# Performance work log

Hardware: AMD Instinct MI355X
Metric: run time of the kernel (lower is better)

## Reference

```python
import jax, jax.numpy as jnp
import numpy as np

EPS = 1e-5  # BatchNorm eps
STRIDE = 10  # front_stride

def conv1d(x, w, b, stride=1, padding=0, dilation=1, groups=1):
    # x: [N,C,T], w: [O, C//groups, K] (torch OIH layout)
    y = jax.lax.conv_general_dilated(
        x, w, (stride,), [(padding, padding)], rhs_dilation=(dilation,),
        dimension_numbers=('NCH', 'OIH', 'NCH'), feature_group_count=groups)
    return y + b[None, :, None]

def bn_eval(x, g, b, m, v):
    scale = g / jnp.sqrt(v + EPS)
    return (x - m[None, :, None]) * scale[None, :, None] + b[None, :, None]

def prelu(x, a):
    return jnp.where(x > 0, x, a * x)

def setup_inputs() -> dict:
    key = jax.random.key(0)
    ks = jax.random.split(key, 12)
    B, Cin, T = 2, 1, 64000
    E, D, BL, L, K, FK = 256, 512, 2, 6, 3, 20
    s = 0.05
    x = jax.random.normal(ks[0], (B, Cin, T), dtype=jnp.float32)
    enc_w = jax.random.normal(ks[1], (E, Cin, FK), dtype=jnp.float32) * s
    enc_b = jnp.zeros((E,), jnp.float32)
    w1 = jax.random.normal(ks[2], (BL, L, D, E, 1), dtype=jnp.float32) * s
    b1 = jnp.zeros((BL, L, D), jnp.float32)
    a1 = jnp.full((BL, L), 0.25, jnp.float32)
    g1 = jnp.ones((BL, L, D), jnp.float32)
    be1 = jnp.zeros((BL, L, D), jnp.float32)
    m1 = jax.random.normal(ks[3], (BL, L, D), dtype=jnp.float32) * 0.1
    v1 = jax.random.uniform(ks[4], (BL, L, D), jnp.float32, 0.5, 1.5)
    wd = jax.random.normal(ks[5], (BL, L, D, 1, K), dtype=jnp.float32) * s
    bd = jnp.zeros((BL, L, D), jnp.float32)
    a2 = jnp.full((BL, L), 0.25, jnp.float32)
    g2 = jnp.ones((BL, L, D), jnp.float32)
    be2 = jnp.zeros((BL, L, D), jnp.float32)
    m2 = jax.random.normal(ks[6], (BL, L, D), dtype=jnp.float32) * 0.1
    v2 = jax.random.uniform(ks[7], (BL, L, D), jnp.float32, 0.5, 1.5)
    w2 = jax.random.normal(ks[8], (BL, L, E, D, 1), dtype=jnp.float32) * s
    b2 = jnp.zeros((BL, L, E), jnp.float32)
    dec_w = jax.random.normal(ks[9], (E, Cin, FK), dtype=jnp.float32) * s
    dec_b = jnp.zeros((Cin,), jnp.float32)
    return dict(x=x, enc_w=enc_w, enc_b=enc_b, w1=w1, b1=b1, a1=a1, g1=g1,
                be1=be1, m1=m1, v1=v1, wd=wd, bd=bd, a2=a2, g2=g2, be2=be2,
                m2=m2, v2=v2, w2=w2, b2=b2, dec_w=dec_w, dec_b=dec_b)

def reference(x, enc_w, enc_b, w1, b1, a1, g1, be1, m1, v1, wd, bd,
              a2, g2, be2, m2, v2, w2, b2, dec_w, dec_b):
    T = x.shape[2]
    FK = enc_w.shape[-1]
    D = wd.shape[2]
    blocks, layers = w1.shape[0], w1.shape[1]
    # encoder: Conv1d(in, E, FK, stride=10, padding=FK)
    enc = conv1d(x, enc_w, enc_b, stride=STRIDE, padding=FK)
    h = enc
    for bI in range(blocks):
        resid = h
        for i in range(layers):
            dil = 2 ** i
            h = conv1d(h, w1[bI, i], b1[bI, i])
            h = bn_eval(prelu(h, a1[bI, i]), g1[bI, i], be1[bI, i], m1[bI, i], v1[bI, i])
            h = conv1d(h, wd[bI, i], bd[bI, i], padding=dil, dilation=dil, groups=D)
            h = bn_eval(prelu(h, a2[bI, i]), g2[bI, i], be2[bI, i], m2[bI, i], v2[bI, i])
            h = conv1d(h, w2[bI, i], b2[bI, i])
        h = h + resid
    mask = jax.nn.sigmoid(h)
    masked = enc * mask
    # ConvTranspose1d(E, in, FK, stride=10, padding=0) as lhs-dilated conv
    wt = jnp.flip(dec_w, -1).transpose(1, 0, 2)  # [in, E, FK]
    dec = jax.lax.conv_general_dilated(
        masked, wt, (1,), [(FK - 1, FK - 1)], lhs_dilation=(STRIDE,),
        dimension_numbers=('NCH', 'OIH', 'NCH')) + dec_b[None, :, None]
    return dec[:, :, FK:T + FK]
```

## Files before the change

kernel.cpp:

```cpp
#include <hip/hip_runtime.h>
#include <math.h>

#define TLEN   64000
#define ECH    256
#define DCH    512
#define NBLK   2
#define NLAY   6
#define FKC    20
#define STRIDE_ 10
#define TC     6403
#define NS     12928
#define NTILE  101
#define EPSV   1e-5f

typedef __attribute__((ext_vector_type(8))) short          s8v;
typedef __attribute__((ext_vector_type(4))) float          f4v;
typedef __attribute__((ext_vector_type(4))) unsigned short u4v;
typedef __attribute__((ext_vector_type(8))) unsigned short u8v;

__device__ __forceinline__ unsigned short f2bf(float f) {
    union { float f; unsigned u; } v; v.f = f;
    unsigned r = v.u + 0x7FFFu + ((v.u >> 16) & 1u);
    return (unsigned short)(r >> 16);
}
__device__ __forceinline__ float bf2f(unsigned short h) {
    union { unsigned u; float f; } v; v.u = ((unsigned)h) << 16; return v.f;
}

#define NWQ (12*512*256/4)
__global__ __launch_bounds__(256)
void wcvt_k(const float* __restrict__ w1, const float* __restrict__ w2,
            unsigned short* __restrict__ w1b, unsigned short* __restrict__ w2b)
{
    int i = blockIdx.x * 256 + threadIdx.x;
    if (i < NWQ) {
        float4 v = ((const float4*)w1)[i];
        u4v o = { f2bf(v.x), f2bf(v.y), f2bf(v.z), f2bf(v.w) };
        ((u4v*)w1b)[i] = o;
    } else {
        int j = i - NWQ;
        float4 v = ((const float4*)w2)[j];
        u4v o = { f2bf(v.x), f2bf(v.y), f2bf(v.z), f2bf(v.w) };
        ((u4v*)w2b)[j] = o;
    }
}

__global__ __launch_bounds__(256)
void encoder_k(const float* __restrict__ x, const float* __restrict__ ew,
               const float* __restrict__ eb,
               unsigned short* __restrict__ EncB, unsigned short* __restrict__ Hb)
{
    __shared__ float xs[660];
    const int bx  = blockIdx.x;
    const int b   = blockIdx.y;
    const int tc0 = bx * 64;
    const int base_g = tc0 * STRIDE_ - FKC;
    for (int i = threadIdx.x; i < 660; i += 256) {
        int idx = base_g + i;
        xs[i] = (idx >= 0 && idx < TLEN) ? x[b * TLEN + idx] : 0.f;
    }
    __syncthreads();

    const int e = threadIdx.x;
    float w[20];
    #pragma unroll
    for (int q = 0; q < 5; ++q) {
        float4 v = *(const float4*)&ew[e * 20 + q * 4];
        w[q*4+0] = v.x; w[q*4+1] = v.y; w[q*4+2] = v.z; w[q*4+3] = v.w;
    }
    const float bz = eb[e];
    const int jmax = (TC - tc0 < 64) ? (TC - tc0) : 64;
    for (int j = 0; j < jmax; ++j) {
        const float* xp = &xs[j * 10];
        float acc = bz;
        #pragma unroll
        for (int k = 0; k < 20; ++k) acc = fmaf(xp[k], w[k], acc);
        unsigned short hv = f2bf(acc);
        size_t o = (size_t)(b * TC + tc0 + j) * 256 + e;
        EncB[o] = hv;
        Hb[o]   = hv;
    }
}

template<int KD, int MOUT, int EPI>
__global__ __launch_bounds__(256)
void gemm_bf16_k(const unsigned short* __restrict__ Wb,
                 const unsigned short* __restrict__ Act,
                 unsigned short* __restrict__ OutB,
                 const float* __restrict__ bias,
                 const float* __restrict__ alpha,
                 const float* __restrict__ gamma,
                 const float* __restrict__ beta,
                 const float* __restrict__ mean,
                 const float* __restrict__ var,
                 const unsigned short* __restrict__ Resid)
{
    __shared__ short At[2 * 128 * 32];
    __shared__ short Bt[2 * 128 * 32];

    const int t    = threadIdx.x;
    const int lane = t & 63;
    const int wid  = t >> 6;
    const int wm   = wid >> 1, wn = wid & 1;
    const int r16  = lane & 15, g = lane >> 4;
    const int mb   = blockIdx.y * 128;
    const int nb   = blockIdx.x * 128;

    f4v acc[4][4];
    #pragma unroll
    for (int a = 0; a < 4; ++a)
        #pragma unroll
        for (int c = 0; c < 4; ++c)
            acc[a][c] = (f4v){0.f, 0.f, 0.f, 0.f};

    const char* gA = (const char*)Wb;
    const char* gB = (const char*)Act;
    char* lA = (char*)At;
    char* lB = (char*)Bt;

    auto stage = [&](int buf, int k0) {
        #pragma unroll
        for (int i = 0; i < 2; ++i) {
            int ch = i * 256 + t;
            const char* srcA = gA + ((size_t)(mb + (ch >> 2)) * KD + k0) * 2 + (ch & 3) * 16;
            __builtin_amdgcn_global_load_lds(
                (const __attribute__((address_space(1))) void*)srcA,
                (__attribute__((address_space(3))) void*)(lA + buf * 8192 + i * 4096 + wid * 1024),
                16, 0, 0);
            const char* srcB = gB + ((size_t)(nb + (ch >> 2)) * KD + k0) * 2 + (ch & 3) * 16;
            __builtin_amdgcn_global_load_lds(
                (const __attribute__((address_space(1))) void*)srcB,
                (__attribute__((address_space(3))) void*)(lB + buf * 8192 + i * 4096 + wid * 1024),
                16, 0, 0);
        }
    };

    constexpr int NSTEP = KD / 32;
    stage(0, 0);
    __syncthreads();

    for (int s = 0; s < NSTEP; ++s) {
        const int cur = s & 1;
        if (s + 1 < NSTEP) stage(cur ^ 1, (s + 1) * 32);

        const short* cA = At + cur * 128 * 32;
        const short* cB = Bt + cur * 128 * 32;
        s8v av[4], bv[4];
        #pragma unroll
        for (int f = 0; f < 4; ++f) {
            av[f] = *(const s8v*)&cA[(wm * 64 + f * 16 + r16) * 32 + g * 8];
            bv[f] = *(const s8v*)&cB[(wn * 64 + f * 16 + r16) * 32 + g * 8];
        }
        #pragma unroll
        for (int fm = 0; fm < 4; ++fm)
            #pragma unroll
            for (int fn = 0; fn < 4; ++fn)
                acc[fm][fn] = __builtin_amdgcn_mfma_f32_16x16x32_bf16(
                    av[fm], bv[fn], acc[fm][fn], 0, 0, 0);

        __syncthreads();
    }

    float al = 0.f;
    if constexpr (EPI == 0) al = alpha[0];
    #pragma unroll
    for (int fm = 0; fm < 4; ++fm) {
        const int mbase = mb + wm * 64 + fm * 16 + g * 4;
        float4 b4 = *(const float4*)&bias[mbase];
        float bb[4] = { b4.x, b4.y, b4.z, b4.w };
        float sc[4], mn[4], bt[4];
        if constexpr (EPI == 0) {
            float4 g4  = *(const float4*)&gamma[mbase];
            float4 v4  = *(const float4*)&var[mbase];
            float4 m4  = *(const float4*)&mean[mbase];
            float4 be4 = *(const float4*)&beta[mbase];
            sc[0] = g4.x / sqrtf(v4.x + EPSV); sc[1] = g4.y / sqrtf(v4.y + EPSV);
            sc[2] = g4.z / sqrtf(v4.z + EPSV); sc[3] = g4.w / sqrtf(v4.w + EPSV);
            mn[0] = m4.x; mn[1] = m4.y; mn[2] = m4.z; mn[3] = m4.w;
            bt[0] = be4.x; bt[1] = be4.y; bt[2] = be4.z; bt[3] = be4.w;
        }
        #pragma unroll
        for (int fn = 0; fn < 4; ++fn) {
            const int n = nb + wn * 64 + fn * 16 + r16;
            f4v a = acc[fm][fn];
            u4v rv = {};
            if constexpr (EPI == 2) rv = *(const u4v*)&Resid[(size_t)n * MOUT + mbase];
            u4v ro;
            #pragma unroll
            for (int r = 0; r < 4; ++r) {
                float v = a[r] + bb[r];
                if constexpr (EPI == 0) {
                    v = (v > 0.f) ? v : al * v;
                    v = (v - mn[r]) * sc[r] + bt[r];
                }
                if constexpr (EPI == 2) v += bf2f(rv[r]);
                ro[r] = f2bf(v);
            }
            *(u4v*)&OutB[(size_t)n * MOUT + mbase] = ro;
        }
    }
}

__global__ __launch_bounds__(256)
void dw_k(const unsigned short* __restrict__ P, const float* __restrict__ wd,
          const float* __restrict__ bd, const float* __restrict__ a2,
          const float* __restrict__ g2, const float* __restrict__ be2,
          const float* __restrict__ m2, const float* __restrict__ v2,
          unsigned short* __restrict__ Q, int dil)
{
    const int t  = threadIdx.x;
    const int d8 = (t & 63) * 8;
    const int n  = blockIdx.x * 4 + (t >> 6);
    const int b  = (n >= TC) ? 1 : 0;
    const int tt = n - b * TC;

    u8v c = *(const u8v*)&P[(size_t)n * 512 + d8];
    u8v l = {}, r = {};
    const bool hasL = (tt - dil >= 0);
    const bool hasR = (tt + dil < TC);
    if (hasL) l = *(const u8v*)&P[(size_t)(n - dil) * 512 + d8];
    if (hasR) r = *(const u8v*)&P[(size_t)(n + dil) * 512 + d8];

    float w24[24];
    #pragma unroll
    for (int q = 0; q < 6; ++q) {
        float4 v = *(const float4*)&wd[d8 * 3 + q * 4];
        w24[q*4+0] = v.x; w24[q*4+1] = v.y; w24[q*4+2] = v.z; w24[q*4+3] = v.w;
    }
    float bdv[8], gv[8], bev[8], mnv[8], vrv[8];
    #pragma unroll
    for (int q = 0; q < 2; ++q) {
        float4 v0 = *(const float4*)&bd[d8 + q*4];
        float4 v1 = *(const float4*)&g2[d8 + q*4];
        float4 v2_ = *(const float4*)&be2[d8 + q*4];
        float4 v3 = *(const float4*)&m2[d8 + q*4];
        float4 v4 = *(const float4*)&v2[d8 + q*4];
        bdv[q*4+0]=v0.x; bdv[q*4+1]=v0.y; bdv[q*4+2]=v0.z; bdv[q*4+3]=v0.w;
        gv [q*4+0]=v1.x; gv [q*4+1]=v1.y; gv [q*4+2]=v1.z; gv [q*4+3]=v1.w;
        bev[q*4+0]=v2_.x;bev[q*4+1]=v2_.y;bev[q*4+2]=v2_.z;bev[q*4+3]=v2_.w;
        mnv[q*4+0]=v3.x; mnv[q*4+1]=v3.y; mnv[q*4+2]=v3.z; mnv[q*4+3]=v3.w;
        vrv[q*4+0]=v4.x; vrv[q*4+1]=v4.y; vrv[q*4+2]=v4.z; vrv[q*4+3]=v4.w;
    }
    const float al = a2[0];

    u8v o;
    #pragma unroll
    for (int i = 0; i < 8; ++i) {
        float acc = bf2f(c[i]) * w24[i*3+1];
        if (hasL) acc = fmaf(bf2f(l[i]), w24[i*3+0], acc);
        if (hasR) acc = fmaf(bf2f(r[i]), w24[i*3+2], acc);
        acc += bdv[i];
        acc = (acc > 0.f) ? acc : al * acc;
        acc = (acc - mnv[i]) * (gv[i] / sqrtf(vrv[i] + EPSV)) + bev[i];
        o[i] = f2bf(acc);
    }
    *(u8v*)&Q[(size_t)n * 512 + d8] = o;
}

#define TOT8 ((ECH * NS) / 8)
__global__ __launch_bounds__(256)
void mask_k(const unsigned short* __restrict__ EncB,
            const unsigned short* __restrict__ Hb,
            unsigned short* __restrict__ Mb)
{
    int i = blockIdx.x * 256 + threadIdx.x;
    u8v ev = ((const u8v*)EncB)[i];
    u8v hv = ((const u8v*)Hb)[i];
    u8v o;
    #pragma unroll
    for (int k = 0; k < 8; ++k) {
        float h = bf2f(hv[k]);
        float s = 1.f / (1.f + expf(-h));
        o[k] = f2bf(bf2f(ev[k]) * s);
    }
    ((u8v*)Mb)[i] = o;
}

__global__ __launch_bounds__(256)
void decoder_k(const unsigned short* __restrict__ Mb,
               const float* __restrict__ dec_w, const float* __restrict__ db,
               float* __restrict__ out)
{
    __shared__ float wlds[5120];
    __shared__ float red[2560];
    const int t = threadIdx.x;
    #pragma unroll
    for (int i = 0; i < 5; ++i)
        ((float4*)wlds)[t + i * 256] = ((const float4*)dec_w)[t + i * 256];
    __syncthreads();

    const int grp = t >> 5;
    const int t0l = t & 31;
    const int t0  = blockIdx.x * 32 + t0l;
    const int by  = blockIdx.y;
    const int n0  = by * TC + t0 + 2;
    const int e0  = grp * 32;

    float acc[10];
    #pragma unroll
    for (int j = 0; j < 10; ++j) acc[j] = 0.f;

    #pragma unroll
    for (int q = 0; q < 4; ++q) {
        u8v a0 = *(const u8v*)&Mb[(size_t)n0 * 256 + e0 + q * 8];
        u8v a1 = *(const u8v*)&Mb[(size_t)(n0 - 1) * 256 + e0 + q * 8];
        #pragma unroll
        for (int i = 0; i < 8; ++i) {
            float m0 = bf2f(a0[i]);
            float m1 = bf2f(a1[i]);
            const float* wr = &wlds[(e0 + q * 8 + i) * 20];
            #pragma unroll
            for (int j = 0; j < 10; ++j)
                acc[j] = fmaf(m0, wr[j], fmaf(m1, wr[j + 10], acc[j]));
        }
    }
    #pragma unroll
    for (int j = 0; j < 10; ++j)
        red[(t0l * 8 + grp) * 10 + j] = acc[j];
    __syncthreads();

    for (int s = t; s < 320; s += 256) {
        int t0l2 = s / 10, j = s - t0l2 * 10;
        float sm = 0.f;
        #pragma unroll
        for (int gq = 0; gq < 8; ++gq) sm += red[(t0l2 * 8 + gq) * 10 + j];
        out[(size_t)by * TLEN + (size_t)(blockIdx.x * 32 + t0l2) * 10 + j] = sm + db[0];
    }
}

extern "C" void kernel_launch(void* const* d_in, const int* in_sizes, int n_in,
                              void* d_out, int out_size, void* d_ws, size_t ws_size,
                              hipStream_t stream)
{
    (void)in_sizes; (void)n_in; (void)out_size; (void)ws_size;
    const float* x     = (const float*)d_in[0];
    const float* enc_w = (const float*)d_in[1];
    const float* enc_b = (const float*)d_in[2];
    const float* w1    = (const float*)d_in[3];
    const float* b1    = (const float*)d_in[4];
    const float* a1    = (const float*)d_in[5];
    const float* g1    = (const float*)d_in[6];
    const float* be1   = (const float*)d_in[7];
    const float* m1    = (const float*)d_in[8];
    const float* v1    = (const float*)d_in[9];
    const float* wd    = (const float*)d_in[10];
    const float* bd    = (const float*)d_in[11];
    const float* a2    = (const float*)d_in[12];
    const float* g2    = (const float*)d_in[13];
    const float* be2   = (const float*)d_in[14];
    const float* m2    = (const float*)d_in[15];
    const float* v2    = (const float*)d_in[16];
    const float* w2    = (const float*)d_in[17];
    const float* b2    = (const float*)d_in[18];
    const float* dec_w = (const float*)d_in[19];
    const float* dec_b = (const float*)d_in[20];
    float* out = (float*)d_out;

    const size_t B_EN = (size_t)NS * 256 * 2;
    const size_t B_DN = (size_t)NS * 512 * 2;
    char* p = (char*)d_ws;
    unsigned short* Hb   = (unsigned short*)p;  p += B_EN;
    unsigned short* Hb2  = (unsigned short*)p;  p += B_EN;
    unsigned short* EncB = (unsigned short*)p;  p += B_EN;
    unsigned short* Pb   = (unsigned short*)p;  p += B_DN;
    unsigned short* Qb   = (unsigned short*)p;  p += B_DN;
    unsigned short* w1b  = (unsigned short*)p;  p += (size_t)12*512*256*2;
    unsigned short* w2b  = (unsigned short*)p;
    unsigned short* Mb   = Pb;

    dim3 blk(256);
    wcvt_k<<<dim3(2 * NWQ / 256), blk, 0, stream>>>(w1, w2, w1b, w2b);
    encoder_k<<<dim3(101, 2), blk, 0, stream>>>(x, enc_w, enc_b, EncB, Hb);

    for (int bI = 0; bI < NBLK; ++bI) {
        for (int i = 0; i < NLAY; ++i) {
            const int li  = bI * NLAY + i;
            const int dil = 1 << i;
            const unsigned short* hin = (i == 0) ? Hb : Hb2;
            gemm_bf16_k<ECH, DCH, 0><<<dim3(NTILE, DCH / 128), blk, 0, stream>>>(
                w1b + (size_t)li * DCH * ECH, hin, Pb,
                b1 + (size_t)li * DCH, a1 + li,
                g1 + (size_t)li * DCH, be1 + (size_t)li * DCH,
                m1 + (size_t)li * DCH, v1 + (size_t)li * DCH, nullptr);
            dw_k<<<dim3(NS / 4), blk, 0, stream>>>(
                Pb, wd + (size_t)li * DCH * 3, bd + (size_t)li * DCH, a2 + li,
                g2 + (size_t)li * DCH, be2 + (size_t)li * DCH,
                m2 + (size_t)li * DCH, v2 + (size_t)li * DCH, Qb, dil);
            if (i == NLAY - 1) {
                gemm_bf16_k<DCH, ECH, 2><<<dim3(NTILE, ECH / 128), blk, 0, stream>>>(
                    w2b + (size_t)li * ECH * DCH, Qb, Hb,
                    b2 + (size_t)li * ECH, nullptr, nullptr, nullptr,
                    nullptr, nullptr, Hb);
            } else {
                gemm_bf16_k<DCH, ECH, 1><<<dim3(NTILE, ECH / 128), blk, 0, stream>>>(
                    w2b + (size_t)li * ECH * DCH, Qb, Hb2,
                    b2 + (size_t)li * ECH, nullptr, nullptr, nullptr,
                    nullptr, nullptr, nullptr);
            }
        }
    }

    mask_k<<<dim3(TOT8 / 256), blk, 0, stream>>>(EncB, Hb, Mb);
    decoder_k<<<dim3(200, 2), blk, 0, stream>>>(Mb, dec_w, dec_b, out);
}
```

Measured before the change: 655.5 us.

## Fuse depthwise conv into second pointwise GEMM and sigmoid mask into last layer

The depthwise dilated conv plus PReLU/BN is now computed on the fly while staging the B operand of the second pointwise GEMM, which removes the Qb intermediate write and read per layer. The sigmoid mask is folded into the final layer's GEMM epilogue, and depthwise parameters are prepacked once into an 8-float record per channel. In exchange, each GEMM block recomputes the depthwise values and loads three neighbour rows. The old double-buffered LDS staging is replaced by a single padded buffer with register prefetch, and the other N-tile block recomputes the same depthwise outputs.

```diff
diff --git a/kernel.cpp b/kernel.cpp
--- a/kernel.cpp
+++ b/kernel.cpp
@@ -28,20 +28,44 @@
 }
 
 #define NWQ (12*512*256/4)
+#define NB0 (2*NWQ/256)
 __global__ __launch_bounds__(256)
 void wcvt_k(const float* __restrict__ w1, const float* __restrict__ w2,
-            unsigned short* __restrict__ w1b, unsigned short* __restrict__ w2b)
-{
-    int i = blockIdx.x * 256 + threadIdx.x;
-    if (i < NWQ) {
-        float4 v = ((const float4*)w1)[i];
-        u4v o = { f2bf(v.x), f2bf(v.y), f2bf(v.z), f2bf(v.w) };
-        ((u4v*)w1b)[i] = o;
+            const float* __restrict__ wd, const float* __restrict__ bd,
+            const float* __restrict__ a2, const float* __restrict__ g2,
+            const float* __restrict__ be2, const float* __restrict__ m2,
+            const float* __restrict__ v2,
+            unsigned short* __restrict__ w1b, unsigned short* __restrict__ w2b,
+            float* __restrict__ dwp)
+{
+    const int bx = blockIdx.x;
+    const int t  = threadIdx.x;
+    if (bx < NB0) {
+        int i = bx * 256 + t;
+        if (i < NWQ) {
+            float4 v = ((const float4*)w1)[i];
+            u4v o = { f2bf(v.x), f2bf(v.y), f2bf(v.z), f2bf(v.w) };
+            ((u4v*)w1b)[i] = o;
+        } else {
+            int j = i - NWQ;
+            float4 v = ((const float4*)w2)[j];
+            u4v o = { f2bf(v.x), f2bf(v.y), f2bf(v.z), f2bf(v.w) };
+            ((u4v*)w2b)[j] = o;
+        }
     } else {
-        int j = i - NWQ;
-        float4 v = ((const float4*)w2)[j];
-        u4v o = { f2bf(v.x), f2bf(v.y), f2bf(v.z), f2bf(v.w) };
-        ((u4v*)w2b)[j] = o;
+        int idx = (bx - NB0) * 256 + t;
+        int li = idx >> 9, d = idx & 511;
+        float w0  = wd[li * 1536 + d * 3 + 0];
+        float w1v = wd[li * 1536 + d * 3 + 1];
+        float w2v = wd[li * 1536 + d * 3 + 2];
+        float bdv = bd[li * 512 + d];
+        float sc  = g2[li * 512 + d] / sqrtf(v2[li * 512 + d] + EPSV);
+        float mn  = m2[li * 512 + d];
+        float bt  = be2[li * 512 + d];
+        float al  = a2[li];
+        float* o = dwp + (size_t)idx * 8;
+        o[0] = w0; o[1] = w1v; o[2] = w2v; o[3] = bdv;
+        o[4] = sc; o[5] = mn;  o[6] = bt;  o[7] = al;
     }
 }
 
@@ -82,7 +106,7 @@
     }
 }
 
-template<int KD, int MOUT, int EPI>
+template<int KD, int MOUT>
 __global__ __launch_bounds__(256)
 void gemm_bf16_k(const unsigned short* __restrict__ Wb,
                  const unsigned short* __restrict__ Act,
@@ -92,8 +116,7 @@
                  const float* __restrict__ gamma,
                  const float* __restrict__ beta,
                  const float* __restrict__ mean,
-                 const float* __restrict__ var,
-                 const unsigned short* __restrict__ Resid)
+                 const float* __restrict__ var)
 {
     __shared__ short At[2 * 128 * 32];
     __shared__ short Bt[2 * 128 * 32];
@@ -161,39 +184,30 @@
         __syncthreads();
     }
 
-    float al = 0.f;
-    if constexpr (EPI == 0) al = alpha[0];
+    const float al = alpha[0];
     #pragma unroll
     for (int fm = 0; fm < 4; ++fm) {
         const int mbase = mb + wm * 64 + fm * 16 + g * 4;
         float4 b4 = *(const float4*)&bias[mbase];
         float bb[4] = { b4.x, b4.y, b4.z, b4.w };
-        float sc[4], mn[4], bt[4];
-        if constexpr (EPI == 0) {
-            float4 g4  = *(const float4*)&gamma[mbase];
-            float4 v4  = *(const float4*)&var[mbase];
-            float4 m4  = *(const float4*)&mean[mbase];
-            float4 be4 = *(const float4*)&beta[mbase];
-            sc[0] = g4.x / sqrtf(v4.x + EPSV); sc[1] = g4.y / sqrtf(v4.y + EPSV);
-            sc[2] = g4.z / sqrtf(v4.z + EPSV); sc[3] = g4.w / sqrtf(v4.w + EPSV);
-            mn[0] = m4.x; mn[1] = m4.y; mn[2] = m4.z; mn[3] = m4.w;
-            bt[0] = be4.x; bt[1] = be4.y; bt[2] = be4.z; bt[3] = be4.w;
-        }
+        float4 g4  = *(const float4*)&gamma[mbase];
+        float4 v4  = *(const float4*)&var[mbase];
+        float4 m4  = *(const float4*)&mean[mbase];
+        float4 be4 = *(const float4*)&beta[mbase];
+        float sc[4] = { g4.x / sqrtf(v4.x + EPSV), g4.y / sqrtf(v4.y + EPSV),
+                        g4.z / sqrtf(v4.z + EPSV), g4.w / sqrtf(v4.w + EPSV) };
+        float mn[4] = { m4.x, m4.y, m4.z, m4.w };
+        float bt[4] = { be4.x, be4.y, be4.z, be4.w };
         #pragma unroll
         for (int fn = 0; fn < 4; ++fn) {
             const int n = nb + wn * 64 + fn * 16 + r16;
             f4v a = acc[fm][fn];
-            u4v rv = {};
-            if constexpr (EPI == 2) rv = *(const u4v*)&Resid[(size_t)n * MOUT + mbase];
             u4v ro;
             #pragma unroll
             for (int r = 0; r < 4; ++r) {
                 float v = a[r] + bb[r];
-                if constexpr (EPI == 0) {
-                    v = (v > 0.f) ? v : al * v;
-                    v = (v - mn[r]) * sc[r] + bt[r];
-                }
-                if constexpr (EPI == 2) v += bf2f(rv[r]);
+                v = (v > 0.f) ? v : al * v;
+                v = (v - mn[r]) * sc[r] + bt[r];
                 ro[r] = f2bf(v);
             }
             *(u4v*)&OutB[(size_t)n * MOUT + mbase] = ro;
@@ -201,79 +215,144 @@
     }
 }
 
+#define LROW2 40
+
+template<int EPI>
 __global__ __launch_bounds__(256)
-void dw_k(const unsigned short* __restrict__ P, const float* __restrict__ wd,
-          const float* __restrict__ bd, const float* __restrict__ a2,
-          const float* __restrict__ g2, const float* __restrict__ be2,
-          const float* __restrict__ m2, const float* __restrict__ v2,
-          unsigned short* __restrict__ Q, int dil)
-{
-    const int t  = threadIdx.x;
-    const int d8 = (t & 63) * 8;
-    const int n  = blockIdx.x * 4 + (t >> 6);
-    const int b  = (n >= TC) ? 1 : 0;
-    const int tt = n - b * TC;
-
-    u8v c = *(const u8v*)&P[(size_t)n * 512 + d8];
-    u8v l = {}, r = {};
-    const bool hasL = (tt - dil >= 0);
-    const bool hasR = (tt + dil < TC);
-    if (hasL) l = *(const u8v*)&P[(size_t)(n - dil) * 512 + d8];
-    if (hasR) r = *(const u8v*)&P[(size_t)(n + dil) * 512 + d8];
-
-    float w24[24];
-    #pragma unroll
-    for (int q = 0; q < 6; ++q) {
-        float4 v = *(const float4*)&wd[d8 * 3 + q * 4];
-        w24[q*4+0] = v.x; w24[q*4+1] = v.y; w24[q*4+2] = v.z; w24[q*4+3] = v.w;
-    }
-    float bdv[8], gv[8], bev[8], mnv[8], vrv[8];
-    #pragma unroll
-    for (int q = 0; q < 2; ++q) {
-        float4 v0 = *(const float4*)&bd[d8 + q*4];
-        float4 v1 = *(const float4*)&g2[d8 + q*4];
-        float4 v2_ = *(const float4*)&be2[d8 + q*4];
-        float4 v3 = *(const float4*)&m2[d8 + q*4];
-        float4 v4 = *(const float4*)&v2[d8 + q*4];
-        bdv[q*4+0]=v0.x; bdv[q*4+1]=v0.y; bdv[q*4+2]=v0.z; bdv[q*4+3]=v0.w;
-        gv [q*4+0]=v1.x; gv [q*4+1]=v1.y; gv [q*4+2]=v1.z; gv [q*4+3]=v1.w;
-        bev[q*4+0]=v2_.x;bev[q*4+1]=v2_.y;bev[q*4+2]=v2_.z;bev[q*4+3]=v2_.w;
-        mnv[q*4+0]=v3.x; mnv[q*4+1]=v3.y; mnv[q*4+2]=v3.z; mnv[q*4+3]=v3.w;
-        vrv[q*4+0]=v4.x; vrv[q*4+1]=v4.y; vrv[q*4+2]=v4.z; vrv[q*4+3]=v4.w;
-    }
-    const float al = a2[0];
-
-    u8v o;
-    #pragma unroll
-    for (int i = 0; i < 8; ++i) {
-        float acc = bf2f(c[i]) * w24[i*3+1];
-        if (hasL) acc = fmaf(bf2f(l[i]), w24[i*3+0], acc);
-        if (hasR) acc = fmaf(bf2f(r[i]), w24[i*3+2], acc);
-        acc += bdv[i];
-        acc = (acc > 0.f) ? acc : al * acc;
-        acc = (acc - mnv[i]) * (gv[i] / sqrtf(vrv[i] + EPSV)) + bev[i];
-        o[i] = f2bf(acc);
-    }
-    *(u8v*)&Q[(size_t)n * 512 + d8] = o;
-}
-
-#define TOT8 ((ECH * NS) / 8)
-__global__ __launch_bounds__(256)
-void mask_k(const unsigned short* __restrict__ EncB,
-            const unsigned short* __restrict__ Hb,
-            unsigned short* __restrict__ Mb)
-{
-    int i = blockIdx.x * 256 + threadIdx.x;
-    u8v ev = ((const u8v*)EncB)[i];
-    u8v hv = ((const u8v*)Hb)[i];
-    u8v o;
-    #pragma unroll
-    for (int k = 0; k < 8; ++k) {
-        float h = bf2f(hv[k]);
-        float s = 1.f / (1.f + expf(-h));
-        o[k] = f2bf(bf2f(ev[k]) * s);
-    }
-    ((u8v*)Mb)[i] = o;
+void gemm_dw_k(const unsigned short* __restrict__ Wb,
+               const unsigned short* __restrict__ Pin,
+               const float* __restrict__ dwpL,
+               unsigned short* __restrict__ OutB,
+               const float* __restrict__ bias,
+               const unsigned short* __restrict__ Resid,
+               const unsigned short* __restrict__ EncB,
+               int dil)
+{
+    constexpr int KD   = DCH;
+    constexpr int MOUT = ECH;
+    __shared__ short At[128 * LROW2];
+    __shared__ short Bt[128 * LROW2];
+
+    const int t    = threadIdx.x;
+    const int lane = t & 63;
+    const int wid  = t >> 6;
+    const int wm   = wid >> 1, wn = wid & 1;
+    const int r16  = lane & 15, g = lane >> 4;
+    const int mb   = blockIdx.y * 128;
+    const int nb   = blockIdx.x * 128;
+
+    const int arow = t >> 2;
+    const int kc8  = (t & 3) * 8;
+
+    const unsigned short* pA0 = &Wb[(size_t)(mb + arow)      * KD + kc8];
+    const unsigned short* pA1 = &Wb[(size_t)(mb + arow + 64) * KD + kc8];
+
+    const int n0r = nb + arow, n1r = n0r + 64;
+    const int b0 = (n0r >= TC) ? 1 : 0, b1 = (n1r >= TC) ? 1 : 0;
+    const int tt0 = n0r - b0 * TC,      tt1 = n1r - b1 * TC;
+    const bool hL0 = (tt0 - dil >= 0), hR0 = (tt0 + dil < TC);
+    const bool hL1 = (tt1 - dil >= 0), hR1 = (tt1 + dil < TC);
+    const unsigned short* pc0 = &Pin[(size_t)n0r * 512 + kc8];
+    const unsigned short* pc1 = &Pin[(size_t)n1r * 512 + kc8];
+    const long doff = (long)dil * 512;
+
+    f4v acc[4][4];
+    #pragma unroll
+    for (int a = 0; a < 4; ++a)
+        #pragma unroll
+        for (int c = 0; c < 4; ++c)
+            acc[a][c] = (f4v){0.f, 0.f, 0.f, 0.f};
+
+    constexpr int NSTEP = KD / 32;
+    s8v a0 = *(const s8v*)pA0, a1 = *(const s8v*)pA1;
+    s8v c0 = *(const s8v*)pc0, c1 = *(const s8v*)pc1;
+    s8v l0 = {}, r0 = {}, l1 = {}, r1 = {};
+    if (hL0) l0 = *(const s8v*)(pc0 - doff);
+    if (hR0) r0 = *(const s8v*)(pc0 + doff);
+    if (hL1) l1 = *(const s8v*)(pc1 - doff);
+    if (hR1) r1 = *(const s8v*)(pc1 + doff);
+
+    for (int s = 0; s < NSTEP; ++s) {
+        const int k0 = s * 32;
+        __syncthreads();
+        *(s8v*)&At[(arow)      * LROW2 + kc8] = a0;
+        *(s8v*)&At[(arow + 64) * LROW2 + kc8] = a1;
+        {
+            s8v ob0, ob1;
+            #pragma unroll
+            for (int j = 0; j < 8; ++j) {
+                const float4 pa = *(const float4*)&dwpL[(size_t)(k0 + kc8 + j) * 8];
+                const float4 pb = *(const float4*)&dwpL[(size_t)(k0 + kc8 + j) * 8 + 4];
+                float a = bf2f(((const unsigned short*)&c0)[j]) * pa.y;
+                if (hL0) a = fmaf(bf2f(((const unsigned short*)&l0)[j]), pa.x, a);
+                if (hR0) a = fmaf(bf2f(((const unsigned short*)&r0)[j]), pa.z, a);
+                a += pa.w;
+                a = (a > 0.f) ? a : pb.w * a;
+                a = (a - pb.y) * pb.x + pb.z;
+                ((unsigned short*)&ob0)[j] = f2bf(a);
+                float e = bf2f(((const unsigned short*)&c1)[j]) * pa.y;
+                if (hL1) e = fmaf(bf2f(((const unsigned short*)&l1)[j]), pa.x, e);
+                if (hR1) e = fmaf(bf2f(((const unsigned short*)&r1)[j]), pa.z, e);
+                e += pa.w;
+                e = (e > 0.f) ? e : pb.w * e;
+                e = (e - pb.y) * pb.x + pb.z;
+                ((unsigned short*)&ob1)[j] = f2bf(e);
+            }
+            *(s8v*)&Bt[(arow)      * LROW2 + kc8] = ob0;
+            *(s8v*)&Bt[(arow + 64) * LROW2 + kc8] = ob1;
+        }
+        __syncthreads();
+
+        const int k0n = ((s + 1 < NSTEP) ? (s + 1) : s) * 32;
+        a0 = *(const s8v*)(pA0 + k0n); a1 = *(const s8v*)(pA1 + k0n);
+        c0 = *(const s8v*)(pc0 + k0n); c1 = *(const s8v*)(pc1 + k0n);
+        if (hL0) l0 = *(const s8v*)(pc0 - doff + k0n);
+        if (hR0) r0 = *(const s8v*)(pc0 + doff + k0n);
+        if (hL1) l1 = *(const s8v*)(pc1 - doff + k0n);
+        if (hR1) r1 = *(const s8v*)(pc1 + doff + k0n);
+
+        s8v av[4], bv[4];
+        #pragma unroll
+        for (int f = 0; f < 4; ++f) {
+            av[f] = *(const s8v*)&At[(wm * 64 + f * 16 + r16) * LROW2 + g * 8];
+            bv[f] = *(const s8v*)&Bt[(wn * 64 + f * 16 + r16) * LROW2 + g * 8];
+        }
+        #pragma unroll
+        for (int fm = 0; fm < 4; ++fm)
+            #pragma unroll
+            for (int fn = 0; fn < 4; ++fn)
+                acc[fm][fn] = __builtin_amdgcn_mfma_f32_16x16x32_bf16(
+                    av[fm], bv[fn], acc[fm][fn], 0, 0, 0);
+    }
+
+    #pragma unroll
+    for (int fm = 0; fm < 4; ++fm) {
+        const int mbase = mb + wm * 64 + fm * 16 + g * 4;
+        float4 b4 = *(const float4*)&bias[mbase];
+        float bb[4] = { b4.x, b4.y, b4.z, b4.w };
+        #pragma unroll
+        for (int fn = 0; fn < 4; ++fn) {
+            const int n = nb + wn * 64 + fn * 16 + r16;
+            f4v a = acc[fm][fn];
+            u4v rv = {}, ev = {};
+            if constexpr (EPI >= 2) rv = *(const u4v*)&Resid[(size_t)n * MOUT + mbase];
+            if constexpr (EPI == 3) ev = *(const u4v*)&EncB[(size_t)n * 256 + mbase];
+            u4v ro;
+            #pragma unroll
+            for (int r = 0; r < 4; ++r) {
+                float v = a[r] + bb[r];
+                if constexpr (EPI >= 2) v += bf2f(rv[r]);
+                if constexpr (EPI == 3) {
+                    float h  = bf2f(f2bf(v));
+                    float sg = 1.f / (1.f + expf(-h));
+                    ro[r] = f2bf(bf2f(ev[r]) * sg);
+                } else {
+                    ro[r] = f2bf(v);
+                }
+            }
+            *(u4v*)&OutB[(size_t)n * MOUT + mbase] = ro;
+        }
+    }
 }
 
 __global__ __launch_bounds__(256)
@@ -365,11 +444,13 @@
     unsigned short* Pb   = (unsigned short*)p;  p += B_DN;
     unsigned short* Qb   = (unsigned short*)p;  p += B_DN;
     unsigned short* w1b  = (unsigned short*)p;  p += (size_t)12*512*256*2;
-    unsigned short* w2b  = (unsigned short*)p;
-    unsigned short* Mb   = Pb;
+    unsigned short* w2b  = (unsigned short*)p;  p += (size_t)12*512*256*2;
+    float*          dwp  = (float*)p;
+    unsigned short* Mb   = Qb;
 
     dim3 blk(256);
-    wcvt_k<<<dim3(2 * NWQ / 256), blk, 0, stream>>>(w1, w2, w1b, w2b);
+    wcvt_k<<<dim3(NB0 + 24), blk, 0, stream>>>(w1, w2, wd, bd, a2, g2, be2, m2, v2,
+                                               w1b, w2b, dwp);
     encoder_k<<<dim3(101, 2), blk, 0, stream>>>(x, enc_w, enc_b, EncB, Hb);
 
     for (int bI = 0; bI < NBLK; ++bI) {
@@ -377,29 +458,26 @@
             const int li  = bI * NLAY + i;
             const int dil = 1 << i;
             const unsigned short* hin = (i == 0) ? Hb : Hb2;
-            gemm_bf16_k<ECH, DCH, 0><<<dim3(NTILE, DCH / 128), blk, 0, stream>>>(
+            gemm_bf16_k<ECH, DCH><<<dim3(NTILE, DCH / 128), blk, 0, stream>>>(
                 w1b + (size_t)li * DCH * ECH, hin, Pb,
                 b1 + (size_t)li * DCH, a1 + li,
                 g1 + (size_t)li * DCH, be1 + (size_t)li * DCH,
-                m1 + (size_t)li * DCH, v1 + (size_t)li * DCH, nullptr);
-            dw_k<<<dim3(NS / 4), blk, 0, stream>>>(
-                Pb, wd + (size_t)li * DCH * 3, bd + (size_t)li * DCH, a2 + li,
-                g2 + (size_t)li * DCH, be2 + (size_t)li * DCH,
-                m2 + (size_t)li * DCH, v2 + (size_t)li * DCH, Qb, dil);
-            if (i == NLAY - 1) {
-                gemm_bf16_k<DCH, ECH, 2><<<dim3(NTILE, ECH / 128), blk, 0, stream>>>(
-                    w2b + (size_t)li * ECH * DCH, Qb, Hb,
-                    b2 + (size_t)li * ECH, nullptr, nullptr, nullptr,
-                    nullptr, nullptr, Hb);
+                m1 + (size_t)li * DCH, v1 + (size_t)li * DCH);
+            const float* dwpL = dwp + (size_t)li * 512 * 8;
+            const unsigned short* wL = w2b + (size_t)li * ECH * DCH;
+            const float* bL = b2 + (size_t)li * ECH;
+            if (li == NBLK * NLAY - 1) {
+                gemm_dw_k<3><<<dim3(NTILE, ECH / 128), blk, 0, stream>>>(
+                    wL, Pb, dwpL, Mb, bL, Hb, EncB, dil);
+            } else if (i == NLAY - 1) {
+                gemm_dw_k<2><<<dim3(NTILE, ECH / 128), blk, 0, stream>>>(
+                    wL, Pb, dwpL, Hb, bL, Hb, nullptr, dil);
             } else {
-                gemm_bf16_k<DCH, ECH, 1><<<dim3(NTILE, ECH / 128), blk, 0, stream>>>(
-                    w2b + (size_t)li * ECH * DCH, Qb, Hb2,
-                    b2 + (size_t)li * ECH, nullptr, nullptr, nullptr,
-                    nullptr, nullptr, nullptr);
+                gemm_dw_k<1><<<dim3(NTILE, ECH / 128), blk, 0, stream>>>(
+                    wL, Pb, dwpL, Hb2, bL, nullptr, nullptr, dil);
             }
         }
     }
 
-    mask_k<<<dim3(TOT8 / 256), blk, 0, stream>>>(EncB, Hb, Mb);
     decoder_k<<<dim3(200, 2), blk, 0, stream>>>(Mb, dec_w, dec_b, out);
 }
```

New measurement: 893.8 us. 1.36x slower.
